# Kernel tuning notes

Hardware: AMD Instinct MI355X
Metric: run time of the kernel (lower is better)

The kernel has to match this reference:

```python
import jax, jax.numpy as jnp
import numpy as np

N, E, B = 20000, 160000, 1024
MDIM, EDIM, H, L, PROP = 64, 16, 128, 4, 1000


def _lin(key, fan_in, fan_out, scale=None):
    s = scale if scale is not None else 1.0 / np.sqrt(fan_in)
    return (jax.random.normal(key, (fan_in, fan_out), jnp.float32) * s)


def setup_inputs() -> dict:
    key = jax.random.key(0)
    ks = iter(jax.random.split(key, 64))
    d = {}
    d["x"] = jax.random.normal(next(ks), (N, MDIM), jnp.float32)
    d["pos"] = jax.random.normal(next(ks), (N, 3), jnp.float32)
    d["edge_attr"] = jax.random.normal(next(ks), (E, EDIM), jnp.float32)
    d["edge_index"] = jax.random.randint(next(ks), (2, E), 0, N)
    d["batch"] = jnp.sort(jax.random.randint(next(ks), (N,), 0, B))
    # EGNN embeddings
    d["emb_in_w"] = _lin(next(ks), MDIM, H); d["emb_in_b"] = jnp.zeros((H,), jnp.float32)
    d["emb_out_w"] = _lin(next(ks), H, H); d["emb_out_b"] = jnp.zeros((H,), jnp.float32)
    # per-layer E_GCL params, stacked over layers
    ein = 2 * H + 1 + EDIM  # [h_row, h_col, radial, edge_attr]
    d["edge_w1"] = jnp.stack([_lin(next(ks), ein, H) for _ in range(L)]); d["edge_b1"] = jnp.zeros((L, H), jnp.float32)
    d["edge_w2"] = jnp.stack([_lin(next(ks), H, H) for _ in range(L)]); d["edge_b2"] = jnp.zeros((L, H), jnp.float32)
    d["node_w1"] = jnp.stack([_lin(next(ks), 2 * H, H) for _ in range(L)]); d["node_b1"] = jnp.zeros((L, H), jnp.float32)
    d["node_w2"] = jnp.stack([_lin(next(ks), H, H) for _ in range(L)]); d["node_b2"] = jnp.zeros((L, H), jnp.float32)
    d["coord_w1"] = jnp.stack([_lin(next(ks), H, H) for _ in range(L)]); d["coord_b1"] = jnp.zeros((L, H), jnp.float32)
    d["coord_w2"] = jnp.stack([_lin(next(ks), H, 1, scale=0.001) for _ in range(L)])  # xavier gain=0.001, no bias
    # end_layers: 2 ResBlocks (Dropout->Linear->SiLU->Linear) + head
    d["res_w1"] = jnp.stack([_lin(next(ks), H, H) for _ in range(2)]); d["res_b1"] = jnp.zeros((2, H), jnp.float32)
    d["res_w2"] = jnp.stack([_lin(next(ks), H, H) for _ in range(2)]); d["res_b2"] = jnp.zeros((2, H), jnp.float32)
    d["head_w"] = _lin(next(ks), H, PROP); d["head_b"] = jnp.zeros((PROP,), jnp.float32)
    return d


def _egnn_forward(x, pos, edge_attr, edge_index, batch,
                  emb_in_w, emb_in_b, emb_out_w, emb_out_b,
                  edge_w1, edge_b1, edge_w2, edge_b2,
                  node_w1, node_b1, node_w2, node_b2,
                  coord_w1, coord_b1, coord_w2,
                  res_w1, res_b1, res_w2, res_b2, head_w, head_b):
    silu = jax.nn.silu
    row, col = edge_index[0], edge_index[1]
    h = x @ emb_in_w + emb_in_b                                   # [N, H]
    # edge in-degree counts for coords_agg='mean' (clamped to >=1)
    cnt = jax.ops.segment_sum(jnp.ones((E, 1), h.dtype), row, num_segments=N)
    cnt = jnp.maximum(cnt, 1.0)
    for l in range(L):
        coord_diff = pos[row] - pos[col]                          # [E, 3]
        radial = jnp.sum(coord_diff * coord_diff, axis=-1, keepdims=True)  # [E, 1]
        # edge model
        e_in = jnp.concatenate([h[row], h[col], radial, edge_attr], axis=-1)
        m = silu(silu(e_in @ edge_w1[l] + edge_b1[l]) @ edge_w2[l] + edge_b2[l])  # [E, H]
        # coord model (coords_agg='mean')
        trans = coord_diff * (silu(m @ coord_w1[l] + coord_b1[l]) @ coord_w2[l])  # [E, 3]
        pos = pos + jax.ops.segment_sum(trans, row, num_segments=N) / cnt
        # node model (residual=True)
        agg = jax.ops.segment_sum(m, row, num_segments=N)         # [N, H]
        n_in = jnp.concatenate([h, agg], axis=-1)
        h = h + (silu(n_in @ node_w1[l] + node_b1[l]) @ node_w2[l] + node_b2[l])
    h = h @ emb_out_w + emb_out_b
    g = jax.ops.segment_max(h, batch, num_segments=B)             # [B, H]
    for r in range(2):
        g = g + (silu(g @ res_w1[r] + res_b1[r]) @ res_w2[r] + res_b2[r])
    return g @ head_w + head_b                                    # [B, PROP]


def reference(x, pos, edge_attr, edge_index, batch,
              emb_in_w, emb_in_b, emb_out_w, emb_out_b,
              edge_w1, edge_b1, edge_w2, edge_b2,
              node_w1, node_b1, node_w2, node_b2,
              coord_w1, coord_b1, coord_w2,
              res_w1, res_b1, res_w2, res_b2, head_w, head_b):
    return _egnn_forward(x, pos, edge_attr, edge_index, batch,
                         emb_in_w, emb_in_b, emb_out_w, emb_out_b,
                         edge_w1, edge_b1, edge_w2, edge_b2,
                         node_w1, node_b1, node_w2, node_b2,
                         coord_w1, coord_b1, coord_w2,
                         res_w1, res_b1, res_w2, res_b2, head_w, head_b)
```

## Files before the change

### kernel.cpp

```cpp
#include <hip/hip_runtime.h>
#include <hip/hip_bf16.h>

#define HD 128
#define PROP 1000
#define NPB  8

typedef float f32x4 __attribute__((ext_vector_type(4)));
typedef short s16x8 __attribute__((ext_vector_type(8)));

__device__ __forceinline__ float silu_f(float v) { return v / (1.0f + __expf(-v)); }

__device__ __forceinline__ unsigned short f2bf(float f) {
    union { __hip_bfloat16 h; unsigned short u; } v;
    v.h = __float2bfloat16(f);
    return v.u;
}
__device__ __forceinline__ unsigned pk2(float a, float b) {
    union { __hip_bfloat162 h; unsigned u; } v;
    v.h = __float22bfloat162_rn(make_float2(a, b));
    return v.u;
}
__device__ __forceinline__ float bf2f_lo(unsigned u) { return __uint_as_float(u << 16); }
__device__ __forceinline__ float bf2f_hi(unsigned u) { return __uint_as_float(u & 0xffff0000u); }
__device__ __forceinline__ float4 ld4(const float* p) { return *(const float4*)p; }


__global__ void counti_kernel(const int* __restrict__ ei, int* __restrict__ cnt, int E) {
    int e = blockIdx.x * 256 + threadIdx.x;
    if (e < E) atomicAdd(&cnt[ei[e]], 1);
}

__global__ __launch_bounds__(1024) void scan_blk(
    const int* __restrict__ cnt, int* __restrict__ excl, int* __restrict__ bsum, int N)
{
    __shared__ int wsum[16], wexc[17];
    const int t = threadIdx.x, lane = t & 63, wid = t >> 6;
    const int gid = blockIdx.x * 1024 + t;
    int v = (gid < N) ? cnt[gid] : 0;
    int incl = v;
    #pragma unroll
    for (int d = 1; d < 64; d <<= 1) {
        int x = __shfl_up(incl, d, 64);
        if (lane >= d) incl += x;
    }
    if (lane == 63) wsum[wid] = incl;
    __syncthreads();
    if (t == 0) {
        int a = 0;
        #pragma unroll
        for (int w2 = 0; w2 < 16; ++w2) { wexc[w2] = a; a += wsum[w2]; }
        wexc[16] = a;
    }
    __syncthreads();
    if (gid < N) excl[gid] = wexc[wid] + incl - v;
    if (t == 0) bsum[blockIdx.x] = wexc[16];
}
__global__ __launch_bounds__(64) void scan_top(int* __restrict__ bsum, int nb) {
    const int lane = threadIdx.x;
    int v = (lane < nb) ? bsum[lane] : 0;
    int incl = v;
    #pragma unroll
    for (int d = 1; d < 64; d <<= 1) {
        int x = __shfl_up(incl, d, 64);
        if (lane >= d) incl += x;
    }
    if (lane < nb) bsum[lane] = incl - v;
}
__global__ void scan_add(const int* __restrict__ excl, const int* __restrict__ bsum,
                         int* __restrict__ rp, int* __restrict__ wp, int N, int E) {
    int gid = blockIdx.x * 256 + threadIdx.x;
    if (gid < N) {
        int r = excl[gid] + bsum[gid >> 10];
        rp[gid] = r; wp[gid] = r;
    }
    if (gid == 0) rp[N] = E;
}

__global__ void scatter_kernel(const int* __restrict__ ei, int* __restrict__ wp,
                               int* __restrict__ perm, int* __restrict__ rows_s,
                               int* __restrict__ cols_s, int E) {
    int e = blockIdx.x * 256 + threadIdx.x;
    if (e < E) {
        int r = ei[e];
        int p = atomicAdd(&wp[r], 1);
        perm[p] = e;
        rows_s[p] = r;
        cols_s[p] = ei[E + e];
    }
}

__global__ void eattr_perm_kernel(const float* __restrict__ eattr, const int* __restrict__ perm,
                                  unsigned short* __restrict__ eperm, int E) {
    int i = blockIdx.x * 256 + threadIdx.x;
    if (i >= E) return;
    const float* src = eattr + (size_t)perm[i] * 16;
    float4 a = ld4(src), b = ld4(src + 4), c = ld4(src + 8), d = ld4(src + 12);
    unsigned short* dst = eperm + (size_t)i * 16;
    *(uint4*)dst       = make_uint4(pk2(a.x, a.y), pk2(a.z, a.w), pk2(b.x, b.y), pk2(b.z, b.w));
    *(uint4*)(dst + 8) = make_uint4(pk2(c.x, c.y), pk2(c.z, c.w), pk2(d.x, d.y), pk2(d.z, d.w));
}

__global__ void prep_w1nc(const float* __restrict__ ew1, unsigned short* __restrict__ dst) {
    int idx = blockIdx.x * 256 + threadIdx.x;
    if (idx >= 4 * 256 * 128) return;
    int k = idx & 127, o2 = (idx >> 7) & 255, l = idx >> 15;
    dst[idx] = f2bf(ew1[((size_t)l * 273 + k + ((o2 >> 7) << 7)) * 128 + (o2 & 127)]);
}
__global__ void prep_wattr(const float* __restrict__ ew1, unsigned short* __restrict__ dst) {
    int idx = blockIdx.x * 256 + threadIdx.x;
    if (idx >= 4 * 128 * 32) return;
    int k = idx & 31, o = (idx >> 5) & 127, l = idx >> 12;
    int ksrc = (k < 16) ? (257 + k) : (k == 16 ? 256 : -1);
    float v = (ksrc >= 0) ? ew1[((size_t)l * 273 + ksrc) * 128 + o] : 0.0f;
    dst[idx] = f2bf(v);
}
__global__ void prep_t(const float* __restrict__ src, unsigned short* __restrict__ dst, int K) {
    int idx = blockIdx.x * 256 + threadIdx.x;
    if (idx >= 4 * 128 * K) return;
    int k = idx % K, o = (idx / K) & 127, l = idx / (K * 128);
    dst[idx] = f2bf(src[((size_t)l * K + k) * 128 + o]);
}
__global__ void prep_t_sig(const float* __restrict__ src, unsigned short* __restrict__ dst) {
    int idx = blockIdx.x * 256 + threadIdx.x;
    if (idx >= 4 * 128 * 128) return;
    int k = idx & 127, o = (idx >> 7) & 127, l = idx >> 14;
    int ks = ((k >> 2) & 7) * 16 + ((k >> 5) << 2) + (k & 3);
    dst[idx] = f2bf(src[((size_t)l * 128 + ks) * 128 + o]);
}
__global__ void prep_wemb(const float* __restrict__ src, unsigned short* __restrict__ dst) {
    int idx = blockIdx.x * 256 + threadIdx.x;
    if (idx >= 128 * 64) return;
    int k = idx & 63, o = idx >> 6;
    dst[idx] = f2bf(src[(size_t)k * 128 + o]);
}

__global__ __launch_bounds__(128) void emb_pre_kernel(
    const float* __restrict__ x, const unsigned short* __restrict__ wembt,
    const float* __restrict__ bemb,
    const unsigned short* __restrict__ w1nc, const float* __restrict__ b1,
    float* __restrict__ h, unsigned short* __restrict__ apre, int N)
{
    __shared__ __align__(16) char s_xt[32 * 128];
    __shared__ __align__(16) char s_h[32 * 256];
    const int tid = threadIdx.x;
    const int lane = tid & 63, wid = tid >> 6;
    const int lr = lane & 15, kg = lane >> 4;
    const int n0 = blockIdx.x * 32 + wid * 16;
    {
        int n16 = lane >> 2, q = lane & 3;
        int nn = min(n0 + n16, N - 1);
        int sw2 = (n16 & 7) << 4;
        char* row = s_xt + (wid * 16 + n16) * 128;
        #pragma unroll
        for (int it = 0; it < 4; ++it) {
            float4 v = ld4(x + (size_t)nn * 64 + q * 16 + it * 4);
            *(uint2*)(row + ((q * 32 + it * 8) ^ sw2)) = make_uint2(pk2(v.x, v.y), pk2(v.z, v.w));
        }
    }
    const int nd = n0 + lr;
    const int sw = (lr & 7) << 4;
    f32x4 acc[8];
    #pragma unroll
    for (int mf = 0; mf < 8; ++mf) acc[mf] = (f32x4){0.f, 0.f, 0.f, 0.f};
    {
        const char* brow = s_xt + (wid * 16 + lr) * 128;
        for (int ks = 0; ks < 2; ++ks) {
            s16x8 b = *(const s16x8*)(brow + ((ks * 64 + kg * 16) ^ sw));
            #pragma unroll
            for (int mf = 0; mf < 8; ++mf) {
                s16x8 a = *(const s16x8*)(wembt + (size_t)(mf * 16 + lr) * 64 + ks * 32 + kg * 8);
                acc[mf] = __builtin_amdgcn_mfma_f32_16x16x32_bf16(a, b, acc[mf], 0, 0, 0);
            }
        }
    }
    char* hrow = s_h + (wid * 16 + lr) * 256;
    #pragma unroll
    for (int mf = 0; mf < 8; ++mf) {
        f32x4 bb = *(const f32x4*)(bemb + mf * 16 + kg * 4);
        float v0 = acc[mf][0] + bb[0];
        float v1 = acc[mf][1] + bb[1];
        float v2 = acc[mf][2] + bb[2];
        float v3 = acc[mf][3] + bb[3];
        if (nd < N) *(f32x4*)(h + (size_t)nd * HD + mf * 16 + kg * 4) = (f32x4){v0, v1, v2, v3};
        *(uint2*)(hrow + ((mf * 32 + kg * 8) ^ sw)) = make_uint2(pk2(v0, v1), pk2(v2, v3));
    }
    f32x4 acc2[16];
    #pragma unroll
    for (int mf = 0; mf < 16; ++mf) acc2[mf] = (f32x4){0.f, 0.f, 0.f, 0.f};
    for (int ks = 0; ks < 4; ++ks) {
        s16x8 b = *(const s16x8*)(hrow + ((ks * 64 + kg * 16) ^ sw));
        #pragma unroll
        for (int mf = 0; mf < 16; ++mf) {
            s16x8 a = *(const s16x8*)(w1nc + (size_t)(mf * 16 + lr) * 128 + ks * 32 + kg * 8);
            acc2[mf] = __builtin_amdgcn_mfma_f32_16x16x32_bf16(a, b, acc2[mf], 0, 0, 0);
        }
    }
    if (nd < N) {
        #pragma unroll
        for (int mf = 0; mf < 16; ++mf) {
            float b0 = 0.f, b1v = 0.f, b2v = 0.f, b3v = 0.f;
            if (mf < 8) {
                f32x4 bb = *(const f32x4*)(b1 + mf * 16 + kg * 4);
                b0 = bb[0]; b1v = bb[1]; b2v = bb[2]; b3v = bb[3];
            }
            int pos = ((mf >> 3) << 7) + kg * 32 + (mf & 7) * 4;
            *(uint2*)(apre + (size_t)nd * 256 + pos) =
                make_uint2(pk2(acc2[mf][0] + b0, acc2[mf][1] + b1v), pk2(acc2[mf][2] + b2v, acc2[mf][3] + b3v));
        }
    }
}

__global__ __launch_bounds__(128) void edge_compute_kernel(
    const float* __restrict__ pos, const unsigned short* __restrict__ apre,
    const unsigned short* __restrict__ eperm,
    const int* __restrict__ rows_s, const int* __restrict__ cols_s,
    const unsigned short* __restrict__ wattr,
    const unsigned short* __restrict__ wt2, const float* __restrict__ b2,
    const unsigned short* __restrict__ cwt1, const float* __restrict__ cb1,
    const float* __restrict__ cw2,
    unsigned short* __restrict__ medge, float* __restrict__ trans, int E)
{
    __shared__ __align__(16) char s_m[2][16 * 256];
    __shared__ __align__(16) char s_g[2][16 * 256];

    int wg = blockIdx.x;
    {
        int nper = gridDim.x >> 3;
        if ((gridDim.x & 7) == 0) wg = (wg & 7) * nper + (wg >> 3);
    }
    const int tid = threadIdx.x;
    const int lane = tid & 63, wid = tid >> 6;
    const int lr = lane & 15, kg = lane >> 4;
    const int i0 = wg * 32 + wid * 16;
    const int i = i0 + lr;
    const bool valid = i < E;
    const int ic = min(i, E - 1);
    const int r = rows_s[ic], c = cols_s[ic];

    {
        int e = lane >> 2, q = lane & 3;
        int ce = cols_s[min(i0 + e, E - 1)];
        const char* src = (const char*)(apre + (size_t)ce * 256 + 128);
        char* dst = s_g[wid] + e * 256;
        int sw2 = (e & 7) << 4;
        #pragma unroll
        for (int it = 0; it < 4; ++it) {
            uint4 v = *(const uint4*)(src + it * 64 + q * 16);
            *(uint4*)(dst + ((it * 64 + q * 16) ^ sw2)) = v;
        }
    }

    float dx = pos[r*3+0] - pos[c*3+0];
    float dy = pos[r*3+1] - pos[c*3+1];
    float dz = pos[r*3+2] - pos[c*3+2];
    float rad = dx*dx + dy*dy + dz*dz;

    union { s16x8 v; unsigned u[4]; } battr;
    if (kg < 2) {
        battr.v = *(const s16x8*)(eperm + (size_t)ic * 16 + kg * 8);
    } else {
        battr.u[0] = (kg == 2) ? pk2(rad, 0.f) : 0u;
        battr.u[1] = 0u; battr.u[2] = 0u; battr.u[3] = 0u;
    }

    uint4 rgq[4];
    {
        const unsigned short* rb = apre + (size_t)r * 256 + kg * 32;
        #pragma unroll
        for (int q = 0; q < 4; ++q) rgq[q] = *(const uint4*)(rb + q * 8);
    }
    uint4 cgq[4];
    {
        const char* g = s_g[wid] + lr * 256;
        int swl = (lr & 7) << 4;
        #pragma unroll
        for (int q = 0; q < 4; ++q)
            cgq[q] = *(const uint4*)(g + ((kg * 64 + q * 16) ^ swl));
    }

    char* mrow = s_m[wid] + lr * 256;
    const int sw = (lr & 7) << 4;

    f32x4 acc[8];
    #pragma unroll
    for (int mf = 0; mf < 8; ++mf) acc[mf] = (f32x4){0.f, 0.f, 0.f, 0.f};
    #pragma unroll
    for (int mf = 0; mf < 8; ++mf) {
        s16x8 a = *(const s16x8*)(wattr + (size_t)(mf * 16 + lr) * 32 + kg * 8);
        acc[mf] = __builtin_amdgcn_mfma_f32_16x16x32_bf16(a, battr.v, acc[mf], 0, 0, 0);
    }
    #pragma unroll
    for (int mf = 0; mf < 8; ++mf) {
        unsigned rlo = ((const unsigned*)&rgq[mf >> 1])[(mf & 1) * 2];
        unsigned rhi = ((const unsigned*)&rgq[mf >> 1])[(mf & 1) * 2 + 1];
        unsigned clo = ((const unsigned*)&cgq[mf >> 1])[(mf & 1) * 2];
        unsigned chi = ((const unsigned*)&cgq[mf >> 1])[(mf & 1) * 2 + 1];
        float v0 = silu_f(acc[mf][0] + bf2f_lo(rlo) + bf2f_lo(clo));
        float v1 = silu_f(acc[mf][1] + bf2f_hi(rlo) + bf2f_hi(clo));
        float v2 = silu_f(acc[mf][2] + bf2f_lo(rhi) + bf2f_lo(chi));
        float v3 = silu_f(acc[mf][3] + bf2f_hi(rhi) + bf2f_hi(chi));
        *(uint2*)(mrow + ((kg * 64 + mf * 8) ^ sw)) = make_uint2(pk2(v0, v1), pk2(v2, v3));
    }

    #pragma unroll
    for (int mf = 0; mf < 8; ++mf) acc[mf] = (f32x4){0.f, 0.f, 0.f, 0.f};
    for (int ks = 0; ks < 4; ++ks) {
        s16x8 b = *(const s16x8*)(mrow + ((ks * 64 + kg * 16) ^ sw));
        #pragma unroll
        for (int mf = 0; mf < 8; ++mf) {
            s16x8 a = *(const s16x8*)(wt2 + (size_t)(mf * 16 + lr) * 128 + ks * 32 + kg * 8);
            acc[mf] = __builtin_amdgcn_mfma_f32_16x16x32_bf16(a, b, acc[mf], 0, 0, 0);
        }
    }
    #pragma unroll
    for (int mf = 0; mf < 8; ++mf) {
        f32x4 bb = *(const f32x4*)(b2 + mf * 16 + kg * 4);
        float v0 = silu_f(acc[mf][0] + bb[0]);
        float v1 = silu_f(acc[mf][1] + bb[1]);
        float v2 = silu_f(acc[mf][2] + bb[2]);
        float v3 = silu_f(acc[mf][3] + bb[3]);
        *(uint2*)(mrow + ((mf * 32 + kg * 8) ^ sw)) = make_uint2(pk2(v0, v1), pk2(v2, v3));
    }

    #pragma unroll
    for (int mf = 0; mf < 8; ++mf) acc[mf] = (f32x4){0.f, 0.f, 0.f, 0.f};
    for (int ks = 0; ks < 4; ++ks) {
        s16x8 b = *(const s16x8*)(mrow + ((ks * 64 + kg * 16) ^ sw));
        #pragma unroll
        for (int mf = 0; mf < 8; ++mf) {
            s16x8 a = *(const s16x8*)(cwt1 + (size_t)(mf * 16 + lr) * 128 + ks * 32 + kg * 8);
            acc[mf] = __builtin_amdgcn_mfma_f32_16x16x32_bf16(a, b, acc[mf], 0, 0, 0);
        }
    }

    {
        int e = lane >> 2, q = lane & 3;
        int ie = i0 + e;
        if (ie < E) {
            const char* src = s_m[wid] + e * 256;
            int sw2 = (e & 7) << 4;
            char* dst = (char*)(medge + (size_t)ie * HD);
            #pragma unroll
            for (int it = 0; it < 4; ++it) {
                uint4 v = *(const uint4*)(src + ((it * 64 + q * 16) ^ sw2));
                *(uint4*)(dst + it * 64 + q * 16) = v;
            }
        }
    }

    float part = 0.f;
    #pragma unroll
    for (int mf = 0; mf < 8; ++mf) {
        f32x4 bb = *(const f32x4*)(cb1 + mf * 16 + kg * 4);
        f32x4 cw = *(const f32x4*)(cw2 + mf * 16 + kg * 4);
        part += silu_f(acc[mf][0] + bb[0]) * cw[0];
        part += silu_f(acc[mf][1] + bb[1]) * cw[1];
        part += silu_f(acc[mf][2] + bb[2]) * cw[2];
        part += silu_f(acc[mf][3] + bb[3]) * cw[3];
    }
    part += __shfl_xor(part, 16, 64);
    part += __shfl_xor(part, 32, 64);
    if (valid && kg == 0)
        *(float4*)(trans + (size_t)i * 4) = make_float4(dx * part, dy * part, dz * part, 0.f);
}

__global__ __launch_bounds__(128) void node_fused_kernel(
    float* __restrict__ h, const unsigned short* __restrict__ medge,
    const float* __restrict__ trans, const int* __restrict__ rp,
    float* __restrict__ pos,
    const unsigned short* __restrict__ nw1t, const float* __restrict__ nb1,
    const unsigned short* __restrict__ nw2t, const float* __restrict__ nb2,
    const unsigned short* __restrict__ w1nc_next, const float* __restrict__ b1_next,
    unsigned short* __restrict__ apre, int N, int has_next)
{
    __shared__ __align__(16) char s_x[32 * 512];
    const int tid = threadIdx.x;
    const int lane = tid & 63, wid = tid >> 6;
    const int lr = lane & 15, kg = lane >> 4;
    const int n0 = blockIdx.x * 32 + wid * 16;
    {
        int n16 = lane >> 2, q = lane & 3;
        int nn = min(n0 + n16, N - 1);
        int sw2 = (n16 & 7) << 4;
        char* row = s_x + (wid * 16 + n16) * 512;
        #pragma unroll
        for (int it = 0; it < 8; ++it) {
            int c2 = q * 32 + it * 4;
            float4 v = ld4(h + (size_t)nn * HD + c2);
            *(uint2*)(row + ((c2 * 2) ^ sw2)) = make_uint2(pk2(v.x, v.y), pk2(v.z, v.w));
        }
        const int s = rp[nn], e2 = rp[nn + 1];
        float a[32];
        #pragma unroll
        for (int t = 0; t < 32; ++t) a[t] = 0.f;
        for (int j = s; j < e2; ++j) {
            const unsigned short* mp = medge + (size_t)j * HD + q * 32;
            #pragma unroll
            for (int v4 = 0; v4 < 4; ++v4) {
                uint4 w = *(const uint4*)(mp + v4 * 8);
                a[v4*8+0] += bf2f_lo(w.x); a[v4*8+1] += bf2f_hi(w.x);
                a[v4*8+2] += bf2f_lo(w.y); a[v4*8+3] += bf2f_hi(w.y);
                a[v4*8+4] += bf2f_lo(w.z); a[v4*8+5] += bf2f_hi(w.z);
                a[v4*8+6] += bf2f_lo(w.w); a[v4*8+7] += bf2f_hi(w.w);
            }
        }
        #pragma unroll
        for (int it2 = 0; it2 < 4; ++it2) {
            uint4 w = make_uint4(pk2(a[it2*8+0], a[it2*8+1]), pk2(a[it2*8+2], a[it2*8+3]),
                                 pk2(a[it2*8+4], a[it2*8+5]), pk2(a[it2*8+6], a[it2*8+7]));
            *(uint4*)(row + ((256 + q * 64 + it2 * 16) ^ sw2)) = w;
        }
        if (q < 3 && n0 + n16 < N) {
            float pa = 0.f;
            for (int j = s; j < e2; ++j) pa += trans[(size_t)j * 4 + q];
            pos[(size_t)(n0 + n16) * 3 + q] += pa / fmaxf((float)(e2 - s), 1.0f);
        }
    }
    const int nd = n0 + lr;
    char* brow = s_x + (wid * 16 + lr) * 512;
    const int sw = (lr & 7) << 4;
    f32x4 acc[8];
    #pragma unroll
    for (int mf = 0; mf < 8; ++mf) acc[mf] = (f32x4){0.f, 0.f, 0.f, 0.f};
    for (int ks = 0; ks < 8; ++ks) {
        s16x8 b = *(const s16x8*)(brow + ((ks * 64 + kg * 16) ^ sw));
        #pragma unroll
        for (int mf = 0; mf < 8; ++mf) {
            s16x8 a = *(const s16x8*)(nw1t + (size_t)(mf * 16 + lr) * 256 + ks * 32 + kg * 8);
            acc[mf] = __builtin_amdgcn_mfma_f32_16x16x32_bf16(a, b, acc[mf], 0, 0, 0);
        }
    }
    #pragma unroll
    for (int mf = 0; mf < 8; ++mf) {
        f32x4 bb = *(const f32x4*)(nb1 + mf * 16 + kg * 4);
        float v0 = silu_f(acc[mf][0] + bb[0]);
        float v1 = silu_f(acc[mf][1] + bb[1]);
        float v2 = silu_f(acc[mf][2] + bb[2]);
        float v3 = silu_f(acc[mf][3] + bb[3]);
        *(uint2*)(brow + ((mf * 32 + kg * 8) ^ sw)) = make_uint2(pk2(v0, v1), pk2(v2, v3));
    }
    #pragma unroll
    for (int mf = 0; mf < 8; ++mf) acc[mf] = (f32x4){0.f, 0.f, 0.f, 0.f};
    for (int ks = 0; ks < 4; ++ks) {
        s16x8 b = *(const s16x8*)(brow + ((ks * 64 + kg * 16) ^ sw));
        #pragma unroll
        for (int mf = 0; mf < 8; ++mf) {
            s16x8 a = *(const s16x8*)(nw2t + (size_t)(mf * 16 + lr) * 128 + ks * 32 + kg * 8);
            acc[mf] = __builtin_amdgcn_mfma_f32_16x16x32_bf16(a, b, acc[mf], 0, 0, 0);
        }
    }
    uint2 hpk[8];
    if (nd < N) {
        #pragma unroll
        for (int mf = 0; mf < 8; ++mf) {
            f32x4 bb = *(const f32x4*)(nb2 + mf * 16 + kg * 4);
            float* hp = h + (size_t)nd * HD + mf * 16 + kg * 4;
            f32x4 hv = *(const f32x4*)hp;
            hv[0] += acc[mf][0] + bb[0];
            hv[1] += acc[mf][1] + bb[1];
            hv[2] += acc[mf][2] + bb[2];
            hv[3] += acc[mf][3] + bb[3];
            *(f32x4*)hp = hv;
            hpk[mf] = make_uint2(pk2(hv[0], hv[1]), pk2(hv[2], hv[3]));
        }
    }
    if (!has_next) return;
    #pragma unroll
    for (int mf = 0; mf < 8; ++mf)
        *(uint2*)(brow + ((mf * 32 + kg * 8) ^ sw)) = hpk[mf];
    f32x4 acc2[16];
    #pragma unroll
    for (int mf = 0; mf < 16; ++mf) acc2[mf] = (f32x4){0.f, 0.f, 0.f, 0.f};
    for (int ks = 0; ks < 4; ++ks) {
        s16x8 b = *(const s16x8*)(brow + ((ks * 64 + kg * 16) ^ sw));
        #pragma unroll
        for (int mf = 0; mf < 16; ++mf) {
            s16x8 a = *(const s16x8*)(w1nc_next + (size_t)(mf * 16 + lr) * 128 + ks * 32 + kg * 8);
            acc2[mf] = __builtin_amdgcn_mfma_f32_16x16x32_bf16(a, b, acc2[mf], 0, 0, 0);
        }
    }
    if (nd < N) {
        #pragma unroll
        for (int mf = 0; mf < 16; ++mf) {
            float b0 = 0.f, b1v = 0.f, b2v = 0.f, b3v = 0.f;
            if (mf < 8) {
                f32x4 bb = *(const f32x4*)(b1_next + mf * 16 + kg * 4);
                b0 = bb[0]; b1v = bb[1]; b2v = bb[2]; b3v = bb[3];
            }
            int pos2 = ((mf >> 3) << 7) + kg * 32 + (mf & 7) * 4;
            *(uint2*)(apre + (size_t)nd * 256 + pos2) =
                make_uint2(pk2(acc2[mf][0] + b0, acc2[mf][1] + b1v), pk2(acc2[mf][2] + b2v, acc2[mf][3] + b3v));
        }
    }
}

__global__ void ginit_kernel(unsigned* __restrict__ g_enc, int n) {
    int i = blockIdx.x * 256 + threadIdx.x;
    if (i < n) g_enc[i] = 0x007FFFFFu;
}

__global__ __launch_bounds__(128) void embout_segmax_kernel(
    const float* __restrict__ h, const float* __restrict__ w, const float* __restrict__ b,
    const int* __restrict__ batch, unsigned* __restrict__ g_enc, int N)
{
    __shared__ __align__(16) float s_x[HD][12];
    const int tid = threadIdx.x;
    const int n0 = blockIdx.x * NPB;
    #pragma unroll
    for (int n = 0; n < NPB; ++n) {
        int nn = min(n0 + n, N - 1);
        s_x[tid][n] = h[(size_t)nn * HD + tid];
    }
    __syncthreads();
    float acc[NPB];
    {
        float bias = b[tid];
        #pragma unroll
        for (int n = 0; n < NPB; ++n) acc[n] = bias;
    }
    for (int k = 0; k < HD; ++k) {
        float wv = w[(size_t)k * HD + tid];
        float4 x0 = ld4(&s_x[k][0]);
        float4 x1 = ld4(&s_x[k][4]);
        acc[0] += x0.x * wv; acc[1] += x0.y * wv; acc[2] += x0.z * wv; acc[3] += x0.w * wv;
        acc[4] += x1.x * wv; acc[5] += x1.y * wv; acc[6] += x1.z * wv; acc[7] += x1.w * wv;
    }
    #pragma unroll
    for (int n = 0; n < NPB; ++n) {
        if (n0 + n < N) {
            unsigned u = __float_as_uint(acc[n]);
            u = (u & 0x80000000u) ? ~u : (u | 0x80000000u);
            atomicMax(&g_enc[(size_t)batch[n0 + n] * HD + tid], u);
        }
    }
}

__global__ __launch_bounds__(128) void resblock_kernel(
    const unsigned* __restrict__ g_enc,
    const float* __restrict__ rw1, const float* __restrict__ rb1,
    const float* __restrict__ rw2, const float* __restrict__ rb2,
    float* __restrict__ g)
{
    __shared__ float s_g[HD];
    __shared__ float s_t[HD];
    const int b = blockIdx.x, j = threadIdx.x;
    unsigned u = g_enc[(size_t)b * HD + j];
    float v = (u & 0x80000000u) ? __uint_as_float(u & 0x7FFFFFFFu) : __uint_as_float(~u);
    s_g[j] = v;
    __syncthreads();
    for (int r = 0; r < 2; ++r) {
        float a1 = rb1[r * HD + j];
        for (int k = 0; k < HD; ++k) a1 += s_g[k] * rw1[(size_t)r * HD * HD + (size_t)k * HD + j];
        s_t[j] = silu_f(a1);
        __syncthreads();
        float a2 = rb2[r * HD + j];
        for (int k = 0; k < HD; ++k) a2 += s_t[k] * rw2[(size_t)r * HD * HD + (size_t)k * HD + j];
        __syncthreads();
        s_g[j] += a2;
        __syncthreads();
    }
    g[(size_t)b * HD + j] = s_g[j];
}

__global__ __launch_bounds__(256) void head_kernel(
    const float* __restrict__ g, const float* __restrict__ hw, const float* __restrict__ hb,
    float* __restrict__ out, int B)
{
    __shared__ __align__(16) float s_g[HD][8];
    const int b0 = blockIdx.y * 8;
    const int p = blockIdx.x * 256 + threadIdx.x;
    for (int t = threadIdx.x; t < 8 * HD; t += 256) {
        int b = t & 7, k = t >> 3;
        s_g[k][b] = g[(size_t)min(b0 + b, B - 1) * HD + k];
    }
    __syncthreads();
    if (p >= PROP) return;
    float hbp = hb[p];
    float acc[8];
    #pragma unroll
    for (int b = 0; b < 8; ++b) acc[b] = hbp;
    for (int k = 0; k < HD; ++k) {
        float w = hw[(size_t)k * PROP + p];
        float4 g0 = *(const float4*)&s_g[k][0];
        float4 g1 = *(const float4*)&s_g[k][4];
        acc[0] += g0.x * w; acc[1] += g0.y * w; acc[2] += g0.z * w; acc[3] += g0.w * w;
        acc[4] += g1.x * w; acc[5] += g1.y * w; acc[6] += g1.z * w; acc[7] += g1.w * w;
    }
    #pragma unroll
    for (int b = 0; b < 8; ++b)
        if (b0 + b < B) out[(size_t)(b0 + b) * PROP + p] = acc[b];
}

extern "C" void kernel_launch(void* const* d_in, const int* in_sizes, int n_in,
                              void* d_out, int out_size, void* d_ws, size_t ws_size,
                              hipStream_t stream)
{
    const float* x        = (const float*)d_in[0];
    const float* pos_in   = (const float*)d_in[1];
    const float* eattr    = (const float*)d_in[2];
    const int*   ei       = (const int*)d_in[3];
    const int*   batch    = (const int*)d_in[4];
    const float* emb_in_w = (const float*)d_in[5];
    const float* emb_in_b = (const float*)d_in[6];
    const float* emb_out_w= (const float*)d_in[7];
    const float* emb_out_b= (const float*)d_in[8];
    const float* ew1 = (const float*)d_in[9];
    const float* eb1 = (const float*)d_in[10];
    const float* ew2 = (const float*)d_in[11];
    const float* eb2 = (const float*)d_in[12];
    const float* nw1 = (const float*)d_in[13];
    const float* nb1 = (const float*)d_in[14];
    const float* nw2 = (const float*)d_in[15];
    const float* nb2 = (const float*)d_in[16];
    const float* cw1 = (const float*)d_in[17];
    const float* cb1 = (const float*)d_in[18];
    const float* cw2 = (const float*)d_in[19];
    const float* rw1 = (const float*)d_in[20];
    const float* rb1 = (const float*)d_in[21];
    const float* rw2 = (const float*)d_in[22];
    const float* rb2 = (const float*)d_in[23];
    const float* hw  = (const float*)d_in[24];
    const float* hb  = (const float*)d_in[25];
    float* out = (float*)d_out;
    (void)ws_size;

    const int N = in_sizes[0] / 64;
    const int E = in_sizes[2] / 16;
    const int B = out_size / PROP;

    float* wsf = (float*)d_ws;
    float* pos_cur = wsf;   wsf += (size_t)N * 3;
    float* h       = wsf;   wsf += (size_t)N * HD;
    float* g       = wsf;   wsf += (size_t)B * HD;
    float* trans   = wsf;   wsf += (size_t)E * 4;
    wsf += (4 - (((size_t)(wsf - (float*)d_ws)) & 3)) & 3;
    unsigned short* apre  = (unsigned short*)wsf;
    unsigned short* eperm = apre  + (size_t)N * 256;
    unsigned short* w1nc  = eperm + (size_t)E * 16;
    unsigned short* wattr = w1nc  + (size_t)4 * 256 * 128;
    unsigned short* wt2   = wattr + (size_t)4 * 128 * 32;
    unsigned short* cwt1  = wt2   + (size_t)4 * 128 * 128;
    unsigned short* nw1t  = cwt1  + (size_t)4 * 128 * 128;
    unsigned short* nw2t  = nw1t  + (size_t)4 * 128 * 256;
    unsigned short* wembt = nw2t  + (size_t)4 * 128 * 128;
    unsigned short* medge = wembt + (size_t)128 * 64;
    int* ip   = (int*)(medge + (size_t)E * HD);
    unsigned* g_enc = (unsigned*)ip;  ip += (size_t)B * HD;
    int* cnt_i = ip;  ip += N;
    int* rp    = ip;  ip += N + 1;
    int* wp    = ip;  ip += N;
    int* excl  = ip;  ip += N;
    int* bsum  = ip;  ip += 64;
    int* perm  = ip;  ip += E;
    int* rows_s= ip;  ip += E;
    int* cols_s= ip;  ip += E;

    prep_w1nc<<<(4 * 256 * 128 + 255) / 256, 256, 0, stream>>>(ew1, w1nc);
    prep_wattr<<<(4 * 128 * 32 + 255) / 256, 256, 0, stream>>>(ew1, wattr);
    prep_t_sig<<<(4 * 128 * 128 + 255) / 256, 256, 0, stream>>>(ew2, wt2);
    prep_t<<<(4 * 128 * 128 + 255) / 256, 256, 0, stream>>>(cw1, cwt1, 128);
    prep_t<<<(4 * 128 * 256 + 255) / 256, 256, 0, stream>>>(nw1, nw1t, 256);
    prep_t<<<(4 * 128 * 128 + 255) / 256, 256, 0, stream>>>(nw2, nw2t, 128);
    prep_wemb<<<(128 * 64 + 255) / 256, 256, 0, stream>>>(emb_in_w, wembt);

    hipMemsetAsync(cnt_i, 0, (size_t)N * sizeof(int), stream);
    counti_kernel<<<(E + 255) / 256, 256, 0, stream>>>(ei, cnt_i, E);
    const int nb = (N + 1023) / 1024;
    scan_blk<<<nb, 1024, 0, stream>>>(cnt_i, excl, bsum, N);
    scan_top<<<1, 64, 0, stream>>>(bsum, nb);
    scan_add<<<(N + 255) / 256, 256, 0, stream>>>(excl, bsum, rp, wp, N, E);
    scatter_kernel<<<(E + 255) / 256, 256, 0, stream>>>(ei, wp, perm, rows_s, cols_s, E);
    eattr_perm_kernel<<<(E + 255) / 256, 256, 0, stream>>>(eattr, perm, eperm, E);

    hipMemcpyAsync(pos_cur, pos_in, (size_t)N * 3 * sizeof(float),
                   hipMemcpyDeviceToDevice, stream);

    const int nblk = (N + 31) / 32;
    emb_pre_kernel<<<nblk, 128, 0, stream>>>(x, wembt, emb_in_b, w1nc, eb1, h, apre, N);
    for (int l = 0; l < 4; ++l) {
        edge_compute_kernel<<<(E + 31) / 32, 128, 0, stream>>>(
            pos_cur, apre, eperm, rows_s, cols_s,
            wattr + (size_t)l * 128 * 32,
            wt2  + (size_t)l * 128 * 128, eb2 + (size_t)l * HD,
            cwt1 + (size_t)l * 128 * 128, cb1 + (size_t)l * HD,
            cw2 + (size_t)l * HD,
            medge, trans, E);
        node_fused_kernel<<<nblk, 128, 0, stream>>>(
            h, medge, trans, rp, pos_cur,
            nw1t + (size_t)l * 128 * 256, nb1 + (size_t)l * HD,
            nw2t + (size_t)l * 128 * 128, nb2 + (size_t)l * HD,
            w1nc + (size_t)(l + 1 < 4 ? l + 1 : 0) * 256 * 128,
            eb1 + (size_t)(l + 1 < 4 ? l + 1 : 0) * HD,
            apre, N, l < 3 ? 1 : 0);
    }

    ginit_kernel<<<(B * HD + 255) / 256, 256, 0, stream>>>(g_enc, B * HD);
    embout_segmax_kernel<<<(N + NPB - 1) / NPB, 128, 0, stream>>>(
        h, emb_out_w, emb_out_b, batch, g_enc, N);
    resblock_kernel<<<B, 128, 0, stream>>>(g_enc, rw1, rb1, rw2, rb2, g);
    head_kernel<<<dim3((PROP + 255) / 256, (B + 7) / 8), 256, 0, stream>>>(g, hw, hb, out, B);
}
```

Before: 678.0 us.

## Use single-wave blocks for edge/node kernels and MFMA for emb_out segmax

Result: slower. 782.2 us (+15.4%).

```diff
diff --git a/kernel.cpp b/kernel.cpp
--- a/kernel.cpp
+++ b/kernel.cpp
@@ -119,6 +119,12 @@
     if (idx >= 4 * 128 * K) return;
     int k = idx % K, o = (idx / K) & 127, l = idx / (K * 128);
     dst[idx] = f2bf(src[((size_t)l * K + k) * 128 + o]);
+}
+__global__ void prep_t1(const float* __restrict__ src, unsigned short* __restrict__ dst) {
+    int idx = blockIdx.x * 256 + threadIdx.x;
+    if (idx >= 128 * 128) return;
+    int k = idx & 127, o = idx >> 7;
+    dst[idx] = f2bf(src[(size_t)k * 128 + o]);
 }
 __global__ void prep_t_sig(const float* __restrict__ src, unsigned short* __restrict__ dst) {
     int idx = blockIdx.x * 256 + threadIdx.x;
@@ -210,7 +216,7 @@
     }
 }
 
-__global__ __launch_bounds__(128) void edge_compute_kernel(
+__global__ __launch_bounds__(64) void edge_compute_kernel(
     const float* __restrict__ pos, const unsigned short* __restrict__ apre,
     const unsigned short* __restrict__ eperm,
     const int* __restrict__ rows_s, const int* __restrict__ cols_s,
@@ -220,18 +226,17 @@
     const float* __restrict__ cw2,
     unsigned short* __restrict__ medge, float* __restrict__ trans, int E)
 {
-    __shared__ __align__(16) char s_m[2][16 * 256];
-    __shared__ __align__(16) char s_g[2][16 * 256];
+    __shared__ __align__(16) char s_m[16 * 256];
+    __shared__ __align__(16) char s_g[16 * 256];
 
     int wg = blockIdx.x;
     {
         int nper = gridDim.x >> 3;
         if ((gridDim.x & 7) == 0) wg = (wg & 7) * nper + (wg >> 3);
     }
-    const int tid = threadIdx.x;
-    const int lane = tid & 63, wid = tid >> 6;
+    const int lane = threadIdx.x;
     const int lr = lane & 15, kg = lane >> 4;
-    const int i0 = wg * 32 + wid * 16;
+    const int i0 = wg * 16;
     const int i = i0 + lr;
     const bool valid = i < E;
     const int ic = min(i, E - 1);
@@ -241,7 +246,7 @@
         int e = lane >> 2, q = lane & 3;
         int ce = cols_s[min(i0 + e, E - 1)];
         const char* src = (const char*)(apre + (size_t)ce * 256 + 128);
-        char* dst = s_g[wid] + e * 256;
+        char* dst = s_g + e * 256;
         int sw2 = (e & 7) << 4;
         #pragma unroll
         for (int it = 0; it < 4; ++it) {
@@ -271,14 +276,14 @@
     }
     uint4 cgq[4];
     {
-        const char* g = s_g[wid] + lr * 256;
+        const char* g = s_g + lr * 256;
         int swl = (lr & 7) << 4;
         #pragma unroll
         for (int q = 0; q < 4; ++q)
             cgq[q] = *(const uint4*)(g + ((kg * 64 + q * 16) ^ swl));
     }
 
-    char* mrow = s_m[wid] + lr * 256;
+    char* mrow = s_m + lr * 256;
     const int sw = (lr & 7) << 4;
 
     f32x4 acc[8];
@@ -337,7 +342,7 @@
         int e = lane >> 2, q = lane & 3;
         int ie = i0 + e;
         if (ie < E) {
-            const char* src = s_m[wid] + e * 256;
+            const char* src = s_m + e * 256;
             int sw2 = (e & 7) << 4;
             char* dst = (char*)(medge + (size_t)ie * HD);
             #pragma unroll
@@ -364,7 +369,7 @@
         *(float4*)(trans + (size_t)i * 4) = make_float4(dx * part, dy * part, dz * part, 0.f);
 }
 
-__global__ __launch_bounds__(128) void node_fused_kernel(
+__global__ __launch_bounds__(64) void node_fused_kernel(
     float* __restrict__ h, const unsigned short* __restrict__ medge,
     const float* __restrict__ trans, const int* __restrict__ rp,
     float* __restrict__ pos,
@@ -373,16 +378,15 @@
     const unsigned short* __restrict__ w1nc_next, const float* __restrict__ b1_next,
     unsigned short* __restrict__ apre, int N, int has_next)
 {
-    __shared__ __align__(16) char s_x[32 * 512];
-    const int tid = threadIdx.x;
-    const int lane = tid & 63, wid = tid >> 6;
+    __shared__ __align__(16) char s_x[16 * 512];
+    const int lane = threadIdx.x;
     const int lr = lane & 15, kg = lane >> 4;
-    const int n0 = blockIdx.x * 32 + wid * 16;
+    const int n0 = blockIdx.x * 16;
     {
         int n16 = lane >> 2, q = lane & 3;
         int nn = min(n0 + n16, N - 1);
         int sw2 = (n16 & 7) << 4;
-        char* row = s_x + (wid * 16 + n16) * 512;
+        char* row = s_x + n16 * 512;
         #pragma unroll
         for (int it = 0; it < 8; ++it) {
             int c2 = q * 32 + it * 4;
@@ -417,7 +421,7 @@
         }
     }
     const int nd = n0 + lr;
-    char* brow = s_x + (wid * 16 + lr) * 512;
+    char* brow = s_x + lr * 512;
     const int sw = (lr & 7) << 4;
     f32x4 acc[8];
     #pragma unroll
@@ -499,38 +503,53 @@
     if (i < n) g_enc[i] = 0x007FFFFFu;
 }
 
-__global__ __launch_bounds__(128) void embout_segmax_kernel(
-    const float* __restrict__ h, const float* __restrict__ w, const float* __restrict__ b,
-    const int* __restrict__ batch, unsigned* __restrict__ g_enc, int N)
+__global__ __launch_bounds__(64) void embout_mfma_kernel(
+    const float* __restrict__ h, const unsigned short* __restrict__ wot,
+    const float* __restrict__ b, const int* __restrict__ batch,
+    unsigned* __restrict__ g_enc, int N)
 {
-    __shared__ __align__(16) float s_x[HD][12];
-    const int tid = threadIdx.x;
-    const int n0 = blockIdx.x * NPB;
-    #pragma unroll
-    for (int n = 0; n < NPB; ++n) {
-        int nn = min(n0 + n, N - 1);
-        s_x[tid][n] = h[(size_t)nn * HD + tid];
-    }
-    __syncthreads();
-    float acc[NPB];
-    {
-        float bias = b[tid];
-        #pragma unroll
-        for (int n = 0; n < NPB; ++n) acc[n] = bias;
-    }
-    for (int k = 0; k < HD; ++k) {
-        float wv = w[(size_t)k * HD + tid];
-        float4 x0 = ld4(&s_x[k][0]);
-        float4 x1 = ld4(&s_x[k][4]);
-        acc[0] += x0.x * wv; acc[1] += x0.y * wv; acc[2] += x0.z * wv; acc[3] += x0.w * wv;
-        acc[4] += x1.x * wv; acc[5] += x1.y * wv; acc[6] += x1.z * wv; acc[7] += x1.w * wv;
-    }
-    #pragma unroll
-    for (int n = 0; n < NPB; ++n) {
-        if (n0 + n < N) {
-            unsigned u = __float_as_uint(acc[n]);
-            u = (u & 0x80000000u) ? ~u : (u | 0x80000000u);
-            atomicMax(&g_enc[(size_t)batch[n0 + n] * HD + tid], u);
+    __shared__ __align__(16) char s_h[16 * 256];
+    const int lane = threadIdx.x;
+    const int lr = lane & 15, kg = lane >> 4;
+    const int n0 = blockIdx.x * 16;
+    {
+        int n16 = lane >> 2, q = lane & 3;
+        int nn = min(n0 + n16, N - 1);
+        int sw2 = (n16 & 7) << 4;
+        char* row = s_h + n16 * 256;
+        #pragma unroll
+        for (int it = 0; it < 8; ++it) {
+            int c2 = q * 32 + it * 4;
+            float4 v = ld4(h + (size_t)nn * HD + c2);
+            *(uint2*)(row + ((c2 * 2) ^ sw2)) = make_uint2(pk2(v.x, v.y), pk2(v.z, v.w));
+        }
+    }
+    const int nd = n0 + lr;
+    const char* brow = s_h + lr * 256;
+    const int sw = (lr & 7) << 4;
+    f32x4 acc[8];
+    #pragma unroll
+    for (int mf = 0; mf < 8; ++mf) acc[mf] = (f32x4){0.f, 0.f, 0.f, 0.f};
+    for (int ks = 0; ks < 4; ++ks) {
+        s16x8 bv = *(const s16x8*)(brow + ((ks * 64 + kg * 16) ^ sw));
+        #pragma unroll
+        for (int mf = 0; mf < 8; ++mf) {
+            s16x8 a = *(const s16x8*)(wot + (size_t)(mf * 16 + lr) * 128 + ks * 32 + kg * 8);
+            acc[mf] = __builtin_amdgcn_mfma_f32_16x16x32_bf16(a, bv, acc[mf], 0, 0, 0);
+        }
+    }
+    if (nd < N) {
+        const int bi = batch[nd];
+        unsigned* dst = g_enc + (size_t)bi * HD + kg * 4;
+        #pragma unroll
+        for (int mf = 0; mf < 8; ++mf) {
+            f32x4 bb = *(const f32x4*)(b + mf * 16 + kg * 4);
+            #pragma unroll
+            for (int j = 0; j < 4; ++j) {
+                unsigned u = __float_as_uint(acc[mf][j] + bb[j]);
+                u = (u & 0x80000000u) ? ~u : (u | 0x80000000u);
+                atomicMax(dst + mf * 16 + j, u);
+            }
         }
     }
 }
@@ -643,7 +662,8 @@
     unsigned short* nw1t  = cwt1  + (size_t)4 * 128 * 128;
     unsigned short* nw2t  = nw1t  + (size_t)4 * 128 * 256;
     unsigned short* wembt = nw2t  + (size_t)4 * 128 * 128;
-    unsigned short* medge = wembt + (size_t)128 * 64;
+    unsigned short* wot   = wembt + (size_t)128 * 64;
+    unsigned short* medge = wot   + (size_t)128 * 128;
     int* ip   = (int*)(medge + (size_t)E * HD);
     unsigned* g_enc = (unsigned*)ip;  ip += (size_t)B * HD;
     int* cnt_i = ip;  ip += N;
@@ -662,6 +682,7 @@
     prep_t<<<(4 * 128 * 256 + 255) / 256, 256, 0, stream>>>(nw1, nw1t, 256);
     prep_t<<<(4 * 128 * 128 + 255) / 256, 256, 0, stream>>>(nw2, nw2t, 128);
     prep_wemb<<<(128 * 64 + 255) / 256, 256, 0, stream>>>(emb_in_w, wembt);
+    prep_t1<<<(128 * 128 + 255) / 256, 256, 0, stream>>>(emb_out_w, wot);
 
     hipMemsetAsync(cnt_i, 0, (size_t)N * sizeof(int), stream);
     counti_kernel<<<(E + 255) / 256, 256, 0, stream>>>(ei, cnt_i, E);
@@ -675,17 +696,17 @@
     hipMemcpyAsync(pos_cur, pos_in, (size_t)N * 3 * sizeof(float),
                    hipMemcpyDeviceToDevice, stream);
 
-    const int nblk = (N + 31) / 32;
-    emb_pre_kernel<<<nblk, 128, 0, stream>>>(x, wembt, emb_in_b, w1nc, eb1, h, apre, N);
+    emb_pre_kernel<<<(N + 31) / 32, 128, 0, stream>>>(x, wembt, emb_in_b, w1nc, eb1, h, apre, N);
+    const int nblk = (N + 15) / 16;
     for (int l = 0; l < 4; ++l) {
-        edge_compute_kernel<<<(E + 31) / 32, 128, 0, stream>>>(
+        edge_compute_kernel<<<(E + 15) / 16, 64, 0, stream>>>(
             pos_cur, apre, eperm, rows_s, cols_s,
             wattr + (size_t)l * 128 * 32,
             wt2  + (size_t)l * 128 * 128, eb2 + (size_t)l * HD,
             cwt1 + (size_t)l * 128 * 128, cb1 + (size_t)l * HD,
             cw2 + (size_t)l * HD,
             medge, trans, E);
-        node_fused_kernel<<<nblk, 128, 0, stream>>>(
+        node_fused_kernel<<<nblk, 64, 0, stream>>>(
             h, medge, trans, rp, pos_cur,
             nw1t + (size_t)l * 128 * 256, nb1 + (size_t)l * HD,
             nw2t + (size_t)l * 128 * 128, nb2 + (size_t)l * HD,
@@ -695,8 +716,7 @@
     }
 
     ginit_kernel<<<(B * HD + 255) / 256, 256, 0, stream>>>(g_enc, B * HD);
-    embout_segmax_kernel<<<(N + NPB - 1) / NPB, 128, 0, stream>>>(
-        h, emb_out_w, emb_out_b, batch, g_enc, N);
+    embout_mfma_kernel<<<nblk, 64, 0, stream>>>(h, wot, emb_out_b, batch, g_enc, N);
     resblock_kernel<<<B, 128, 0, stream>>>(g_enc, rw1, rb1, rw2, rb2, g);
     head_kernel<<<dim3((PROP + 255) / 256, (B + 7) / 8), 256, 0, stream>>>(g, hw, hb, out, B);
 }
```
